# Kernel optimization log

Measured on AMD Instinct MI355X. Metric: run time of the kernel, lower is better.

## Reference

```python
import jax, jax.numpy as jnp
import numpy as np

EPS = 1e-6

def wave_repr(x, global_mode):
    # x: [B,S,D]
    x = jnp.clip(x, -10.0, 10.0)
    xsq = x * x
    if global_mode:
        Gsq = jnp.sum(xsq, axis=(1, 2), keepdims=True) + EPS  # [B,1,1]
    else:
        Gsq = jnp.sum(xsq, axis=1, keepdims=True) + EPS       # [B,1,D]
    G = jnp.maximum(jnp.sqrt(Gsq), EPS)
    # NOTE: source uses torch.div(..., rounding_mode='floor') -> floor division
    ratio = jnp.clip(jnp.floor(x / G), -0.99, 0.99)
    sqrt_term = jnp.sqrt(jnp.maximum(1.0 - ratio * ratio, EPS))
    alpha = jnp.arctan2(sqrt_term, ratio)
    return G * jnp.cos(alpha), G * jnp.sin(alpha)

def gelu(x):
    return jax.nn.gelu(x, approximate=False)

def rmsnorm(x, w):
    return x * jax.lax.rsqrt(jnp.mean(x * x, axis=-1, keepdims=True) + EPS) * w

def setup_inputs() -> dict:
    key = jax.random.key(0)
    B, S, D = 4, 4096, 1024
    ks = jax.random.split(key, 16)
    s = 0.02
    p = {
        'x': jax.random.normal(ks[0], (B, S, D), jnp.float32),
        'Wa': jax.random.normal(ks[1], (D, D)) * s, 'ba': jnp.zeros((D,)),
        'Wp': jax.random.normal(ks[2], (D, D)) * s, 'bp': jnp.zeros((D,)),
        'gate_bias': jnp.zeros((D,)),
        'w1r': jax.random.normal(ks[3], (D, 4 * D)) * s, 'b1r': jnp.zeros((4 * D,)),
        'w2r': jax.random.normal(ks[4], (4 * D, D)) * s, 'b2r': jnp.zeros((D,)),
        'w1i': jax.random.normal(ks[5], (D, 4 * D)) * s, 'b1i': jnp.zeros((4 * D,)),
        'w2i': jax.random.normal(ks[6], (4 * D, D)) * s, 'b2i': jnp.zeros((D,)),
        'We': jax.random.normal(ks[7], (2 * D, D)) * s, 'be': jnp.zeros((D,)),
        'g_rms': jnp.ones((D,)),
        'wf1': jax.random.normal(ks[8], (D, 2 * D)) * s, 'bf1': jnp.zeros((2 * D,)),
        'wf2': jax.random.normal(ks[9], (2 * D, D)) * s, 'bf2': jnp.zeros((D,)),
    }
    return p

def reference(x, Wa, ba, Wp, bp, gate_bias, w1r, b1r, w2r, b2r, w1i, b1i, w2i, b2i, We, be, g_rms, wf1, bf1, wf2, bf2):
    # wave representations: global (sentence) + local (token)
    rs, is_ = wave_repr(x, True)
    rt, it = wave_repr(x, False)
    cr = rs + rt
    ci = is_ + it
    # amplitude / phase
    amp = jnp.sqrt(cr * cr + ci * ci + EPS)
    ph = jnp.arctan2(ci, cr)
    # biological noise gate (eval mode: no noise)
    gate = jax.nn.sigmoid(amp @ Wa + ba + ph @ Wp + bp + gate_bias)
    gr = cr * gate
    gi = ci * gate
    rp = gelu(gr @ w1r + b1r) @ w2r + b2r
    ip = gelu(gi @ w1i + b1i) @ w2i + b2i
    # combine to embedding + RMSNorm
    wave = jnp.concatenate([rp, ip], axis=-1) @ We + be
    out = rmsnorm(wave, g_rms)
    y = gelu(out @ wf1 + bf1) @ wf2 + bf2
    return y
```

## Files before the change

### kernel.cpp

```cpp
#include <hip/hip_runtime.h>
#include <cmath>

typedef _Float16 f16;
typedef _Float16 f16x8 __attribute__((ext_vector_type(8)));
typedef _Float16 f16x4 __attribute__((ext_vector_type(4)));
typedef float f32x4 __attribute__((ext_vector_type(4)));

#define EPSF 1e-6f

__device__ __forceinline__ void gload16(const f16* g, const f16* l) {
  __builtin_amdgcn_global_load_lds(
      (__attribute__((address_space(1))) void*)g,
      (__attribute__((address_space(3))) void*)l, 16, 0, 0);
}

__device__ __forceinline__ float fast_gelu(float u) {
  const float z = u * 0.70710678118654752f;
  const float az = fabsf(z);
  const float t = __builtin_amdgcn_rcpf(fmaf(0.3275911f, az, 1.0f));
  float p = 1.061405429f;
  p = fmaf(p, t, -1.453152027f);
  p = fmaf(p, t, 1.421413741f);
  p = fmaf(p, t, -0.284496736f);
  p = fmaf(p, t, 0.254829592f);
  p = p * t;
  const float e = __expf(-az * az);
  float er = fmaf(-p, e, 1.0f);
  er = copysignf(er, z);
  return 0.5f * u * (1.0f + er);
}

__global__ void wtr_k(const float* __restrict__ W, f16* __restrict__ WT, int K, int N) {
  __shared__ float t[32][33];
  const int nb = blockIdx.x * 32, kb = blockIdx.y * 32;
  const int tx = threadIdx.x, ty = threadIdx.y;
#pragma unroll
  for (int i = ty; i < 32; i += 8) t[i][tx] = W[(size_t)(kb + i) * N + nb + tx];
  __syncthreads();
#pragma unroll
  for (int i = ty; i < 32; i += 8) WT[(size_t)(nb + i) * K + kb + tx] = (f16)t[tx][i];
}

__global__ void cast_k(const float* __restrict__ W, f16* __restrict__ H) {
  const size_t i = (size_t)blockIdx.x * 256 + threadIdx.x;
  const float4 v = ((const float4*)W)[i];
  f16x4 o;
  o[0] = (f16)v.x; o[1] = (f16)v.y; o[2] = (f16)v.z; o[3] = (f16)v.w;
  ((f16x4*)H)[i] = o;
}

__global__ void colsq_k(const float* __restrict__ x, float* __restrict__ part) {
  const int d = blockIdx.x * 256 + threadIdx.x;
  const int sb = blockIdx.y;
  const int b = blockIdx.z;
  const float* p = x + ((size_t)b * 4096 + (size_t)sb * 256) * 1024 + d;
  float acc = 0.f;
#pragma unroll 4
  for (int s = 0; s < 256; ++s) {
    float v = p[(size_t)s * 1024];
    v = fminf(fmaxf(v, -10.f), 10.f);
    acc = fmaf(v, v, acc);
  }
  part[((size_t)b * 16 + sb) * 1024 + d] = acc;
}

__global__ void stats_k(const float* __restrict__ part, float* __restrict__ Gsum,
                        float* __restrict__ amp) {
  const int b = blockIdx.x;
  const int t = threadIdx.x;
  __shared__ double red[256];
  float cs[4];
  double tot = 0.0;
#pragma unroll
  for (int i = 0; i < 4; ++i) {
    const int d = t + i * 256;
    double s = 0.0;
    for (int k = 0; k < 16; ++k) s += (double)part[((size_t)b * 16 + k) * 1024 + d];
    cs[i] = (float)s;
    tot += s;
  }
  red[t] = tot;
  __syncthreads();
  for (int st = 128; st > 0; st >>= 1) {
    if (t < st) red[t] += red[t + st];
    __syncthreads();
  }
  const float Gs = fmaxf(sqrtf((float)red[0] + EPSF), EPSF);
#pragma unroll
  for (int i = 0; i < 4; ++i) {
    const int d = t + i * 256;
    const float Gt = fmaxf(sqrtf(cs[i] + EPSF), EPSF);
    const float gs = Gs + Gt;
    Gsum[(b << 10) + d] = gs;
    amp[(b << 10) + d] = sqrtf(gs * gs + EPSF);
  }
}

__global__ void rowterm_k(const float* __restrict__ amp, const float* __restrict__ Wa,
                          const float* __restrict__ ba, const float* __restrict__ bp,
                          const float* __restrict__ gbias, float* __restrict__ rt) {
  const int b = blockIdx.y;
  const int d = blockIdx.x * 256 + threadIdx.x;
  const float* a = amp + (b << 10);
  double acc = 0.0;
  for (int k = 0; k < 1024; ++k) acc += (double)a[k] * (double)Wa[((size_t)k << 10) + d];
  rt[(b << 10) + d] = (float)acc + ba[d] + bp[d] + gbias[d];
}

__global__ void bc_k(const float* __restrict__ b2r, const float* __restrict__ b2i,
                     const float* __restrict__ We, const float* __restrict__ be,
                     float* __restrict__ bc) {
  const int n = blockIdx.x * 256 + threadIdx.x;
  double a = 0.0;
  for (int j = 0; j < 1024; ++j) a += (double)b2r[j] * (double)We[(size_t)j * 1024 + n];
  for (int j = 0; j < 1024; ++j)
    a += (double)b2i[j] * (double)We[(size_t)(1024 + j) * 1024 + n];
  bc[n] = (float)a + be[n];
}

__global__ void ph_k(const float* __restrict__ x, f16* __restrict__ ph, float phPos,
                     float phNeg) {
  const size_t i = (size_t)blockIdx.x * 256 + threadIdx.x;
  const float4 v = ((const float4*)x)[i];
  f16x4 o;
  o[0] = (f16)(v.x < 0.f ? phNeg : phPos);
  o[1] = (f16)(v.y < 0.f ? phNeg : phPos);
  o[2] = (f16)(v.z < 0.f ? phNeg : phPos);
  o[3] = (f16)(v.w < 0.f ? phNeg : phPos);
  ((f16x4*)ph)[i] = o;
}

__global__ void rms_k(const float* __restrict__ wave, const float* __restrict__ g,
                      f16* __restrict__ o) {
  const size_t row = blockIdx.x;
  const int t = threadIdx.x;
  const float4 v = ((const float4*)(wave + row * 1024))[t];
  float ss = v.x * v.x + v.y * v.y + v.z * v.z + v.w * v.w;
#pragma unroll
  for (int s = 32; s > 0; s >>= 1) ss += __shfl_down(ss, s);
  __shared__ float red[4];
  if ((t & 63) == 0) red[t >> 6] = ss;
  __syncthreads();
  const float tot = red[0] + red[1] + red[2] + red[3];
  const float r = rsqrtf(tot * (1.f / 1024.f) + EPSF);
  const float4 gv = ((const float4*)g)[t];
  f16x4 ov;
  ov[0] = (f16)(v.x * r * gv.x);
  ov[1] = (f16)(v.y * r * gv.y);
  ov[2] = (f16)(v.z * r * gv.z);
  ov[3] = (f16)(v.w * r * gv.w);
  ((f16x4*)(o + row * 1024))[t] = ov;
}

template <int EPI>
__global__ __launch_bounds__(512, 4) void gemm2_k(
    const f16* __restrict__ A, int lda, const f16* __restrict__ BT, int ldb, int K,
    const float* __restrict__ bias, float* __restrict__ outF, f16* __restrict__ outH,
    int ldo, const f16* __restrict__ phm, const float* __restrict__ rowterm,
    const float* __restrict__ Gsum, f16* __restrict__ gr, f16* __restrict__ gi, int r0,
    float ratioNeg, float stNeg) {
  __shared__ __align__(16) char smem[49152];
  f16(*smA)[4096] = reinterpret_cast<f16(*)[4096]>(smem);
  f16(*smB)[8192] = reinterpret_cast<f16(*)[8192]>(smem + 16384);
  const int tid = threadIdx.x;
  const int w = tid >> 6, l = tid & 63;

  const int ncol = gridDim.y;
  const int bid = blockIdx.x * ncol + blockIdx.y;
  const int nwg = gridDim.x * ncol;
  const int q = nwg >> 3, rr = nwg & 7;
  const int xcd = bid & 7, idx = bid >> 3;
  const int swz = (xcd < rr ? xcd * (q + 1) : rr * (q + 1) + (xcd - rr) * q) + idx;
  const int bx = swz / ncol, by = swz % ncol;
  const size_t rbase = (size_t)bx * 128;
  const size_t cbase = (size_t)by * 256;

  const int srow = (w << 4) + (l >> 2);
  const int slot = l & 3;
  const int ssA = ((slot ^ ((srow >> 1) & 3)) << 3);

  f32x4 acc[4][4];
  const f32x4 zero = {0.f, 0.f, 0.f, 0.f};
#pragma unroll
  for (int m = 0; m < 4; ++m)
#pragma unroll
    for (int n = 0; n < 4; ++n) acc[m][n] = zero;

  const f16* gA = A + (rbase + srow) * (size_t)lda + ssA;
  const f16* gB0 = BT + (cbase + srow) * (size_t)ldb + ssA;
  const int srow1 = srow + 128;
  const f16* gB1 = BT + (cbase + srow1) * (size_t)ldb + ((slot ^ ((srow1 >> 1) & 3)) << 3);

  const int nk = K >> 5;
  auto stage = [&](int buf, size_t ko) {
    gload16(gA + ko, &smA[buf][w << 9]);
    gload16(gB0 + ko, &smB[buf][w << 9]);
    gload16(gB1 + ko, &smB[buf][4096 + (w << 9)]);
  };
  stage(0, 0);
  __syncthreads();

  const int arow = l & 15;
  const int kg = (((l >> 4) ^ ((arow >> 1) & 3)) << 3);
  const int wr = (w >> 2) << 6;
  const int wc = (w & 3) << 6;

  for (int t = 0; t < nk; ++t) {
    const int cur = t & 1;
    if (t + 1 < nk) stage(cur ^ 1, (size_t)(t + 1) << 5);
    const f16* ap = &smA[cur][(wr + arow) * 32 + kg];
    const f16* bp = &smB[cur][(wc + arow) * 32 + kg];
    f16x8 af[4], bf[4];
#pragma unroll
    for (int m = 0; m < 4; ++m) af[m] = *(const f16x8*)(ap + m * 512);
#pragma unroll
    for (int n = 0; n < 4; ++n) bf[n] = *(const f16x8*)(bp + n * 512);
#pragma unroll
    for (int m = 0; m < 4; ++m)
#pragma unroll
      for (int n = 0; n < 4; ++n)
        acc[m][n] = __builtin_amdgcn_mfma_f32_16x16x32_f16(af[m], bf[n], acc[m][n], 0, 0, 0);
    __syncthreads();
  }

  const int fr = l & 15, hi = l >> 4;
  const int r4 = hi << 2;

  if constexpr (EPI == 3 || EPI == 5) {
    float* ep = reinterpret_cast<float*>(smem + w * 4352);
#pragma unroll
    for (int m = 0; m < 4; ++m) {
#pragma unroll
      for (int n = 0; n < 4; ++n) {
        const int cl = n * 16 + fr;
#pragma unroll
        for (int j = 0; j < 4; ++j) {
          float v = acc[m][n][j];
          if constexpr (EPI == 3) v = fast_gelu(v + bias[cbase + wc + cl]);
          ep[(r4 + j) * 68 + cl] = v;
        }
      }
      asm volatile("s_waitcnt lgkmcnt(0)" ::: "memory");
      __builtin_amdgcn_sched_barrier(0);
#pragma unroll
      for (int it = 0; it < 2; ++it) {
        const int rl = l >> 2;
        const int ch = (l & 3) + it * 4;
        const float* pr = &ep[rl * 68 + ch * 8];
        f16x8 o;
#pragma unroll
        for (int e = 0; e < 8; ++e) o[e] = (f16)pr[e];
        *(f16x8*)&outH[(rbase + wr + m * 16 + rl) * (size_t)ldo + (cbase + wc + ch * 8)] = o;
      }
      asm volatile("s_waitcnt lgkmcnt(0)" ::: "memory");
      __builtin_amdgcn_sched_barrier(0);
    }
  } else {
#pragma unroll
    for (int m = 0; m < 4; ++m) {
#pragma unroll
      for (int n = 0; n < 4; ++n) {
        const size_t col = cbase + wc + n * 16 + fr;
#pragma unroll
        for (int j = 0; j < 4; ++j) {
          const size_t row = rbase + wr + m * 16 + r4 + j;
          const float v = acc[m][n][j];
          if constexpr (EPI == 0) {
            outF[row * (size_t)ldo + col] = v + bias[col];
          } else if constexpr (EPI == 1) {
            outF[row * (size_t)ldo + col] += v;
          } else if constexpr (EPI == 4) {
            const int gb = (int)(((size_t)r0 + row) >> 12);
            const float pre = v + rowterm[((size_t)gb << 10) + col];
            const float gate = __builtin_amdgcn_rcpf(1.f + __expf(-pre));
            const float ph = (float)phm[row * 1024 + col];
            const bool neg = ph > 2.f;
            const float gs = Gsum[((size_t)gb << 10) + col];
            const float cr = neg ? gs * ratioNeg : 0.f;
            const float ci = gs * (neg ? stNeg : 1.f);
            gr[row * 1024 + col] = (f16)(cr * gate);
            gi[row * 1024 + col] = (f16)(ci * gate);
          }
        }
      }
    }
  }
}

extern "C" void kernel_launch(void* const* d_in, const int* in_sizes, int n_in,
                              void* d_out, int out_size, void* d_ws, size_t ws_size,
                              hipStream_t stream) {
  const float* x     = (const float*)d_in[0];
  const float* Wa    = (const float*)d_in[1];
  const float* ba    = (const float*)d_in[2];
  const float* Wp    = (const float*)d_in[3];
  const float* bp    = (const float*)d_in[4];
  const float* gbias = (const float*)d_in[5];
  const float* w1r   = (const float*)d_in[6];
  const float* b1r   = (const float*)d_in[7];
  const float* w2r   = (const float*)d_in[8];
  const float* b2r   = (const float*)d_in[9];
  const float* w1i   = (const float*)d_in[10];
  const float* b1i   = (const float*)d_in[11];
  const float* w2i   = (const float*)d_in[12];
  const float* b2i   = (const float*)d_in[13];
  const float* We    = (const float*)d_in[14];
  const float* be    = (const float*)d_in[15];
  const float* grms  = (const float*)d_in[16];
  const float* wf1   = (const float*)d_in[17];
  const float* bf1   = (const float*)d_in[18];
  const float* wf2   = (const float*)d_in[19];
  const float* bf2   = (const float*)d_in[20];
  float* out = (float*)d_out;

  char* ws = (char*)d_ws;
  size_t off = 0;
  auto alloc = [&](size_t bytes) -> void* {
    void* p = (void*)(ws + off);
    off += (bytes + 255) & ~(size_t)255;
    return p;
  };

  f16* WpT   = (f16*)alloc((size_t)1024 * 1024 * 2);
  f16* w1rT  = (f16*)alloc((size_t)4096 * 1024 * 2);
  f16* w1iT  = (f16*)alloc((size_t)4096 * 1024 * 2);
  f16* wf1T  = (f16*)alloc((size_t)2048 * 1024 * 2);
  f16* wf2T  = (f16*)alloc((size_t)1024 * 2048 * 2);
  f16* WcrT  = (f16*)alloc((size_t)1024 * 4096 * 2);
  f16* WciT  = (f16*)alloc((size_t)1024 * 4096 * 2);
  float* part    = (float*)alloc((size_t)4 * 16 * 1024 * 4);
  float* GsumB   = (float*)alloc((size_t)4 * 1024 * 4);
  float* ampB    = (float*)alloc((size_t)4 * 1024 * 4);
  float* rowterm = (float*)alloc((size_t)4 * 1024 * 4);
  float* bcB     = (float*)alloc((size_t)1024 * 4);
  const size_t staticEnd = off;

  char* tmp = ws + staticEnd;
  f16* WeT  = (f16*)tmp;
  f16* w2rH = (f16*)(tmp + (size_t)4 * 1024 * 1024);
  f16* w2iH = (f16*)(tmp + (size_t)12 * 1024 * 1024);

  {
    dim3 b(32, 8);
    wtr_k<<<dim3(32, 32), b, 0, stream>>>(Wp, WpT, 1024, 1024);
    wtr_k<<<dim3(128, 32), b, 0, stream>>>(w1r, w1rT, 1024, 4096);
    wtr_k<<<dim3(128, 32), b, 0, stream>>>(w1i, w1iT, 1024, 4096);
    wtr_k<<<dim3(64, 32), b, 0, stream>>>(wf1, wf1T, 1024, 2048);
    wtr_k<<<dim3(32, 64), b, 0, stream>>>(wf2, wf2T, 2048, 1024);
    wtr_k<<<dim3(32, 64), b, 0, stream>>>(We, WeT, 2048, 1024);
    cast_k<<<dim3(4096), 256, 0, stream>>>(w2r, w2rH);
    cast_k<<<dim3(4096), 256, 0, stream>>>(w2i, w2iH);
  }

  colsq_k<<<dim3(4, 16, 4), 256, 0, stream>>>(x, part);
  stats_k<<<4, 256, 0, stream>>>(part, GsumB, ampB);
  rowterm_k<<<dim3(4, 4), 256, 0, stream>>>(ampB, Wa, ba, bp, gbias, rowterm);
  bc_k<<<dim3(4), 256, 0, stream>>>(b2r, b2i, We, be, bcB);

  gemm2_k<5><<<dim3(8, 16), 512, 0, stream>>>(WeT, 2048, w2rH, 1024, 1024, nullptr,
      nullptr, WcrT, 4096, nullptr, nullptr, nullptr, nullptr, nullptr, 0, 0.f, 0.f);
  gemm2_k<5><<<dim3(8, 16), 512, 0, stream>>>(WeT + 1024, 2048, w2iH, 1024, 1024, nullptr,
      nullptr, WciT, 4096, nullptr, nullptr, nullptr, nullptr, nullptr, 0, 0.f, 0.f);

  const float ratioNeg = -0.99f;
  const float stNeg = sqrtf(fmaxf(1.0f - 0.99f * 0.99f, EPSF));
  const float phPos = atan2f(1.0f, 0.0f);
  const float phNeg = atan2f(stNeg, ratioNeg);

  const long Ntok = (long)in_sizes[0] / 1024;
  const size_t perRow = 14336;
  long R = (long)((ws_size > staticEnd ? ws_size - staticEnd : 0) / perRow);
  R &= ~255L;
  if (R > 8192) R = 8192;
  if (R < 256) R = 256;

  char* cb = ws + staticEnd;
  f16* phB = (f16*)cb;
  f16* grB = (f16*)(cb + (size_t)R * 2048);
  f16* giB = (f16*)(cb + (size_t)R * 4096);
  f16* h1B = (f16*)(cb + (size_t)R * 6144);
  float* waveF = (float*)phB;
  f16* outB = giB;
  f16* h2B = h1B;

  for (long r0 = 0; r0 < Ntok; r0 += R) {
    const long Rc = (Ntok - r0 < R) ? (Ntok - r0) : R;
    const int gm = (int)(Rc / 128);
    ph_k<<<dim3((int)Rc), 256, 0, stream>>>(x + r0 * 1024, phB, phPos, phNeg);
    gemm2_k<4><<<dim3(gm, 4), 512, 0, stream>>>(phB, 1024, WpT, 1024, 1024, nullptr,
        nullptr, nullptr, 1024, phB, rowterm, GsumB, grB, giB, (int)r0, ratioNeg, stNeg);
    gemm2_k<3><<<dim3(gm, 16), 512, 0, stream>>>(grB, 1024, w1rT, 1024, 1024, b1r,
        nullptr, h1B, 4096, nullptr, nullptr, nullptr, nullptr, nullptr, 0, 0.f, 0.f);
    gemm2_k<0><<<dim3(gm, 4), 512, 0, stream>>>(h1B, 4096, WcrT, 4096, 4096, bcB,
        waveF, nullptr, 1024, nullptr, nullptr, nullptr, nullptr, nullptr, 0, 0.f, 0.f);
    gemm2_k<3><<<dim3(gm, 16), 512, 0, stream>>>(giB, 1024, w1iT, 1024, 1024, b1i,
        nullptr, h1B, 4096, nullptr, nullptr, nullptr, nullptr, nullptr, 0, 0.f, 0.f);
    gemm2_k<1><<<dim3(gm, 4), 512, 0, stream>>>(h1B, 4096, WciT, 4096, 4096, nullptr,
        waveF, nullptr, 1024, nullptr, nullptr, nullptr, nullptr, nullptr, 0, 0.f, 0.f);
    rms_k<<<dim3((int)Rc), 256, 0, stream>>>(waveF, grms, outB);
    gemm2_k<3><<<dim3(gm, 8), 512, 0, stream>>>(outB, 1024, wf1T, 1024, 1024, bf1,
        nullptr, h2B, 2048, nullptr, nullptr, nullptr, nullptr, nullptr, 0, 0.f, 0.f);
    gemm2_k<0><<<dim3(gm, 4), 512, 0, stream>>>(h2B, 2048, wf2T, 2048, 2048, bf2,
        out + r0 * 1024, nullptr, 1024, nullptr, nullptr, nullptr, nullptr, nullptr, 0, 0.f, 0.f);
  }
}
```

Before: 1.368 ms.

## Use 128x128-tile GEMM for N=1024 outputs and split-K the small row-term matvecs

Adds a second GEMM kernel with 128x128 tiles and 256 threads, used for every GEMM whose output width is 1024 (gate, the two wave projections, final FFN). This doubles the workgroup count on those launches so the GPU is better filled. The gate epilogue now goes through LDS so the gr/gi stores are vectorized. The serial double-precision matvecs for the row term and the combined bias are split over K into partial kernels plus reduce kernels, which raises parallelism at the cost of extra launches and scratch buffers. The smaller tiles lower per-block data reuse.

New measurement: 1.487 ms. +8.7%, slower.

```diff
diff --git a/kernel.cpp b/kernel.cpp
--- a/kernel.cpp
+++ b/kernel.cpp
@@ -96,26 +96,49 @@
   }
 }
 
-__global__ void rowterm_k(const float* __restrict__ amp, const float* __restrict__ Wa,
-                          const float* __restrict__ ba, const float* __restrict__ bp,
-                          const float* __restrict__ gbias, float* __restrict__ rt) {
+__global__ void rtp_k(const float* __restrict__ amp, const float* __restrict__ Wa,
+                      double* __restrict__ part) {
+  const int d = blockIdx.x * 256 + threadIdx.x;
   const int b = blockIdx.y;
-  const int d = blockIdx.x * 256 + threadIdx.x;
+  const int kc = blockIdx.z;
   const float* a = amp + (b << 10);
   double acc = 0.0;
-  for (int k = 0; k < 1024; ++k) acc += (double)a[k] * (double)Wa[((size_t)k << 10) + d];
+  for (int jj = 0; jj < 128; ++jj) {
+    const int k = kc * 128 + jj;
+    acc += (double)a[k] * (double)Wa[((size_t)k << 10) + d];
+  }
+  part[(((size_t)b * 8 + kc) << 10) + d] = acc;
+}
+__global__ void rtr_k(const double* __restrict__ part, const float* __restrict__ ba,
+                      const float* __restrict__ bp, const float* __restrict__ gbias,
+                      float* __restrict__ rt) {
+  const int d = blockIdx.x * 256 + threadIdx.x;
+  const int b = blockIdx.y;
+  double acc = 0.0;
+#pragma unroll
+  for (int kc = 0; kc < 8; ++kc) acc += part[(((size_t)b * 8 + kc) << 10) + d];
   rt[(b << 10) + d] = (float)acc + ba[d] + bp[d] + gbias[d];
 }
 
-__global__ void bc_k(const float* __restrict__ b2r, const float* __restrict__ b2i,
-                     const float* __restrict__ We, const float* __restrict__ be,
-                     float* __restrict__ bc) {
+__global__ void bcp_k(const float* __restrict__ b2r, const float* __restrict__ b2i,
+                      const float* __restrict__ We, double* __restrict__ part) {
   const int n = blockIdx.x * 256 + threadIdx.x;
-  double a = 0.0;
-  for (int j = 0; j < 1024; ++j) a += (double)b2r[j] * (double)We[(size_t)j * 1024 + n];
-  for (int j = 0; j < 1024; ++j)
-    a += (double)b2i[j] * (double)We[(size_t)(1024 + j) * 1024 + n];
-  bc[n] = (float)a + be[n];
+  const int kc = blockIdx.y;
+  double acc = 0.0;
+  for (int jj = 0; jj < 128; ++jj) {
+    const int j = kc * 128 + jj;
+    const float bv = (j < 1024) ? b2r[j] : b2i[j - 1024];
+    acc += (double)bv * (double)We[(size_t)j * 1024 + n];
+  }
+  part[((size_t)kc << 10) + n] = acc;
+}
+__global__ void bcr_k(const double* __restrict__ part, const float* __restrict__ be,
+                      float* __restrict__ bc) {
+  const int n = blockIdx.x * 256 + threadIdx.x;
+  double acc = 0.0;
+#pragma unroll
+  for (int kc = 0; kc < 16; ++kc) acc += part[((size_t)kc << 10) + n];
+  bc[n] = (float)acc + be[n];
 }
 
 __global__ void ph_k(const float* __restrict__ x, f16* __restrict__ ph, float phPos,
@@ -155,10 +178,7 @@
 template <int EPI>
 __global__ __launch_bounds__(512, 4) void gemm2_k(
     const f16* __restrict__ A, int lda, const f16* __restrict__ BT, int ldb, int K,
-    const float* __restrict__ bias, float* __restrict__ outF, f16* __restrict__ outH,
-    int ldo, const f16* __restrict__ phm, const float* __restrict__ rowterm,
-    const float* __restrict__ Gsum, f16* __restrict__ gr, f16* __restrict__ gi, int r0,
-    float ratioNeg, float stNeg) {
+    const float* __restrict__ bias, f16* __restrict__ outH, int ldo) {
   __shared__ __align__(16) char smem[49152];
   f16(*smA)[4096] = reinterpret_cast<f16(*)[4096]>(smem);
   f16(*smB)[8192] = reinterpret_cast<f16(*)[8192]>(smem + 16384);
@@ -177,7 +197,7 @@
 
   const int srow = (w << 4) + (l >> 2);
   const int slot = l & 3;
-  const int ssA = ((slot ^ ((srow >> 1) & 3)) << 3);
+  const int ss = ((slot ^ ((srow >> 1) & 3)) << 3);
 
   f32x4 acc[4][4];
   const f32x4 zero = {0.f, 0.f, 0.f, 0.f};
@@ -186,10 +206,9 @@
 #pragma unroll
     for (int n = 0; n < 4; ++n) acc[m][n] = zero;
 
-  const f16* gA = A + (rbase + srow) * (size_t)lda + ssA;
-  const f16* gB0 = BT + (cbase + srow) * (size_t)ldb + ssA;
-  const int srow1 = srow + 128;
-  const f16* gB1 = BT + (cbase + srow1) * (size_t)ldb + ((slot ^ ((srow1 >> 1) & 3)) << 3);
+  const f16* gA = A + (rbase + srow) * (size_t)lda + ss;
+  const f16* gB0 = BT + (cbase + srow) * (size_t)ldb + ss;
+  const f16* gB1 = BT + (cbase + srow + 128) * (size_t)ldb + ss;
 
   const int nk = K >> 5;
   auto stage = [&](int buf, size_t ko) {
@@ -225,35 +244,153 @@
 
   const int fr = l & 15, hi = l >> 4;
   const int r4 = hi << 2;
-
-  if constexpr (EPI == 3 || EPI == 5) {
-    float* ep = reinterpret_cast<float*>(smem + w * 4352);
+  float* ep = reinterpret_cast<float*>(smem + w * 4352);
+#pragma unroll
+  for (int m = 0; m < 4; ++m) {
+#pragma unroll
+    for (int n = 0; n < 4; ++n) {
+      const int cl = n * 16 + fr;
+#pragma unroll
+      for (int j = 0; j < 4; ++j) {
+        float v = acc[m][n][j];
+        if constexpr (EPI == 3) v = fast_gelu(v + bias[cbase + wc + cl]);
+        ep[(r4 + j) * 68 + cl] = v;
+      }
+    }
+    asm volatile("s_waitcnt lgkmcnt(0)" ::: "memory");
+    __builtin_amdgcn_sched_barrier(0);
+#pragma unroll
+    for (int it = 0; it < 2; ++it) {
+      const int rl = l >> 2;
+      const int ch = (l & 3) + it * 4;
+      const float* pr = &ep[rl * 68 + ch * 8];
+      f16x8 o;
+#pragma unroll
+      for (int e = 0; e < 8; ++e) o[e] = (f16)pr[e];
+      *(f16x8*)&outH[(rbase + wr + m * 16 + rl) * (size_t)ldo + (cbase + wc + ch * 8)] = o;
+    }
+    asm volatile("s_waitcnt lgkmcnt(0)" ::: "memory");
+    __builtin_amdgcn_sched_barrier(0);
+  }
+}
+
+template <int EPI>
+__global__ __launch_bounds__(256, 5) void gemm1_k(
+    const f16* __restrict__ A, int lda, const f16* __restrict__ BT, int ldb, int K,
+    const float* __restrict__ bias, float* __restrict__ outF, int ldo,
+    const f16* __restrict__ phm, const float* __restrict__ rowterm,
+    const float* __restrict__ Gsum, f16* __restrict__ gr, f16* __restrict__ gi, int r0,
+    float ratioNeg, float stNeg) {
+  __shared__ __align__(16) char smem[32768];
+  f16(*smA)[4096] = reinterpret_cast<f16(*)[4096]>(smem);
+  f16(*smB)[4096] = reinterpret_cast<f16(*)[4096]>(smem + 16384);
+  const int tid = threadIdx.x;
+  const int wv = tid >> 6, ln = tid & 63;
+
+  const int ncol = gridDim.y;
+  const int bid = blockIdx.x * ncol + blockIdx.y;
+  const int nwg = gridDim.x * ncol;
+  const int q = nwg >> 3, rr = nwg & 7;
+  const int xcd = bid & 7, idx = bid >> 3;
+  const int swz = (xcd < rr ? xcd * (q + 1) : rr * (q + 1) + (xcd - rr) * q) + idx;
+  const int bx = swz / ncol, by = swz % ncol;
+  const size_t rbase = (size_t)bx * 128;
+  const size_t cbase = (size_t)by * 128;
+
+  const int srow = (wv << 4) + (ln >> 2);
+  const int slot = ln & 3;
+  const int ss = ((slot ^ ((srow >> 1) & 3)) << 3);
+
+  f32x4 acc[4][4];
+  const f32x4 zero = {0.f, 0.f, 0.f, 0.f};
+#pragma unroll
+  for (int m = 0; m < 4; ++m)
+#pragma unroll
+    for (int n = 0; n < 4; ++n) acc[m][n] = zero;
+
+  const f16* gA = A + (rbase + srow) * (size_t)lda + ss;
+  const f16* gB = BT + (cbase + srow) * (size_t)ldb + ss;
+
+  const int nk = K >> 5;
+  auto stage = [&](int buf, size_t ko) {
+    gload16(gA + ko, &smA[buf][wv << 9]);
+    gload16(gA + ko + (size_t)64 * lda, &smA[buf][2048 + (wv << 9)]);
+    gload16(gB + ko, &smB[buf][wv << 9]);
+    gload16(gB + ko + (size_t)64 * ldb, &smB[buf][2048 + (wv << 9)]);
+  };
+  stage(0, 0);
+  __syncthreads();
+
+  const int arow = ln & 15;
+  const int kg = (((ln >> 4) ^ ((arow >> 1) & 3)) << 3);
+  const int wr = (wv >> 1) << 6;
+  const int wc = (wv & 1) << 6;
+
+  for (int t = 0; t < nk; ++t) {
+    const int cur = t & 1;
+    if (t + 1 < nk) stage(cur ^ 1, (size_t)(t + 1) << 5);
+    const f16* ap = &smA[cur][(wr + arow) * 32 + kg];
+    const f16* bp = &smB[cur][(wc + arow) * 32 + kg];
+    f16x8 af[4], bf[4];
+#pragma unroll
+    for (int m = 0; m < 4; ++m) af[m] = *(const f16x8*)(ap + m * 512);
+#pragma unroll
+    for (int n = 0; n < 4; ++n) bf[n] = *(const f16x8*)(bp + n * 512);
+#pragma unroll
+    for (int m = 0; m < 4; ++m)
+#pragma unroll
+      for (int n = 0; n < 4; ++n)
+        acc[m][n] = __builtin_amdgcn_mfma_f32_16x16x32_f16(af[m], bf[n], acc[m][n], 0, 0, 0);
+    __syncthreads();
+  }
+
+  const int fr = ln & 15, hi = ln >> 4;
+  const int r4 = hi << 2;
+
+  if constexpr (EPI == 4) {
+    float* ep = reinterpret_cast<float*>(smem + wv * 4352);
 #pragma unroll
     for (int m = 0; m < 4; ++m) {
+      float grv[4][4], giv[4][4];
 #pragma unroll
       for (int n = 0; n < 4; ++n) {
-        const int cl = n * 16 + fr;
+        const size_t col = cbase + wc + n * 16 + fr;
 #pragma unroll
         for (int j = 0; j < 4; ++j) {
-          float v = acc[m][n][j];
-          if constexpr (EPI == 3) v = fast_gelu(v + bias[cbase + wc + cl]);
-          ep[(r4 + j) * 68 + cl] = v;
+          const size_t row = rbase + wr + m * 16 + r4 + j;
+          const int gb = (int)(((size_t)r0 + row) >> 12);
+          const float pre = acc[m][n][j] + rowterm[((size_t)gb << 10) + col];
+          const float gate = __builtin_amdgcn_rcpf(1.f + __expf(-pre));
+          const float ph = (float)phm[row * 1024 + col];
+          const bool neg = ph > 2.f;
+          const float gs = Gsum[((size_t)gb << 10) + col];
+          grv[n][j] = (neg ? gs * ratioNeg : 0.f) * gate;
+          giv[n][j] = gs * (neg ? stNeg : 1.f) * gate;
         }
       }
-      asm volatile("s_waitcnt lgkmcnt(0)" ::: "memory");
-      __builtin_amdgcn_sched_barrier(0);
-#pragma unroll
-      for (int it = 0; it < 2; ++it) {
-        const int rl = l >> 2;
-        const int ch = (l & 3) + it * 4;
-        const float* pr = &ep[rl * 68 + ch * 8];
-        f16x8 o;
-#pragma unroll
-        for (int e = 0; e < 8; ++e) o[e] = (f16)pr[e];
-        *(f16x8*)&outH[(rbase + wr + m * 16 + rl) * (size_t)ldo + (cbase + wc + ch * 8)] = o;
+#pragma unroll
+      for (int pass = 0; pass < 2; ++pass) {
+        f16* dst = pass ? gi : gr;
+#pragma unroll
+        for (int n = 0; n < 4; ++n)
+#pragma unroll
+          for (int j = 0; j < 4; ++j)
+            ep[(r4 + j) * 68 + n * 16 + fr] = pass ? giv[n][j] : grv[n][j];
+        asm volatile("s_waitcnt lgkmcnt(0)" ::: "memory");
+        __builtin_amdgcn_sched_barrier(0);
+#pragma unroll
+        for (int it = 0; it < 2; ++it) {
+          const int rl = ln >> 2;
+          const int ch = (ln & 3) + it * 4;
+          const float* pr = &ep[rl * 68 + ch * 8];
+          f16x8 o;
+#pragma unroll
+          for (int e = 0; e < 8; ++e) o[e] = (f16)pr[e];
+          *(f16x8*)&dst[(rbase + wr + m * 16 + rl) * 1024 + (cbase + wc + ch * 8)] = o;
+        }
+        asm volatile("s_waitcnt lgkmcnt(0)" ::: "memory");
+        __builtin_amdgcn_sched_barrier(0);
       }
-      asm volatile("s_waitcnt lgkmcnt(0)" ::: "memory");
-      __builtin_amdgcn_sched_barrier(0);
     }
   } else {
 #pragma unroll
@@ -267,19 +404,8 @@
           const float v = acc[m][n][j];
           if constexpr (EPI == 0) {
             outF[row * (size_t)ldo + col] = v + bias[col];
-          } else if constexpr (EPI == 1) {
+          } else {
             outF[row * (size_t)ldo + col] += v;
-          } else if constexpr (EPI == 4) {
-            const int gb = (int)(((size_t)r0 + row) >> 12);
-            const float pre = v + rowterm[((size_t)gb << 10) + col];
-            const float gate = __builtin_amdgcn_rcpf(1.f + __expf(-pre));
-            const float ph = (float)phm[row * 1024 + col];
-            const bool neg = ph > 2.f;
-            const float gs = Gsum[((size_t)gb << 10) + col];
-            const float cr = neg ? gs * ratioNeg : 0.f;
-            const float ci = gs * (neg ? stNeg : 1.f);
-            gr[row * 1024 + col] = (f16)(cr * gate);
-            gi[row * 1024 + col] = (f16)(ci * gate);
           }
         }
       }
@@ -333,6 +459,8 @@
   float* ampB    = (float*)alloc((size_t)4 * 1024 * 4);
   float* rowterm = (float*)alloc((size_t)4 * 1024 * 4);
   float* bcB     = (float*)alloc((size_t)1024 * 4);
+  double* rtPart = (double*)alloc((size_t)4 * 8 * 1024 * 8);
+  double* bcPart = (double*)alloc((size_t)16 * 1024 * 8);
   const size_t staticEnd = off;
 
   char* tmp = ws + staticEnd;
@@ -354,13 +482,15 @@
 
   colsq_k<<<dim3(4, 16, 4), 256, 0, stream>>>(x, part);
   stats_k<<<4, 256, 0, stream>>>(part, GsumB, ampB);
-  rowterm_k<<<dim3(4, 4), 256, 0, stream>>>(ampB, Wa, ba, bp, gbias, rowterm);
-  bc_k<<<dim3(4), 256, 0, stream>>>(b2r, b2i, We, be, bcB);
+  rtp_k<<<dim3(4, 4, 8), 256, 0, stream>>>(ampB, Wa, rtPart);
+  rtr_k<<<dim3(4, 4), 256, 0, stream>>>(rtPart, ba, bp, gbias, rowterm);
+  bcp_k<<<dim3(4, 16), 256, 0, stream>>>(b2r, b2i, We, bcPart);
+  bcr_k<<<dim3(4), 256, 0, stream>>>(bcPart, be, bcB);
 
   gemm2_k<5><<<dim3(8, 16), 512, 0, stream>>>(WeT, 2048, w2rH, 1024, 1024, nullptr,
-      nullptr, WcrT, 4096, nullptr, nullptr, nullptr, nullptr, nullptr, 0, 0.f, 0.f);
+      WcrT, 4096);
   gemm2_k<5><<<dim3(8, 16), 512, 0, stream>>>(WeT + 1024, 2048, w2iH, 1024, 1024, nullptr,
-      nullptr, WciT, 4096, nullptr, nullptr, nullptr, nullptr, nullptr, 0, 0.f, 0.f);
+      WciT, 4096);
 
   const float ratioNeg = -0.99f;
   const float stNeg = sqrtf(fmaxf(1.0f - 0.99f * 0.99f, EPSF));
@@ -387,20 +517,20 @@
     const long Rc = (Ntok - r0 < R) ? (Ntok - r0) : R;
     const int gm = (int)(Rc / 128);
     ph_k<<<dim3((int)Rc), 256, 0, stream>>>(x + r0 * 1024, phB, phPos, phNeg);
-    gemm2_k<4><<<dim3(gm, 4), 512, 0, stream>>>(phB, 1024, WpT, 1024, 1024, nullptr,
-        nullptr, nullptr, 1024, phB, rowterm, GsumB, grB, giB, (int)r0, ratioNeg, stNeg);
+    gemm1_k<4><<<dim3(gm, 8), 256, 0, stream>>>(phB, 1024, WpT, 1024, 1024, nullptr,
+        nullptr, 1024, phB, rowterm, GsumB, grB, giB, (int)r0, ratioNeg, stNeg);
     gemm2_k<3><<<dim3(gm, 16), 512, 0, stream>>>(grB, 1024, w1rT, 1024, 1024, b1r,
-        nullptr, h1B, 4096, nullptr, nullptr, nullptr, nullptr, nullptr, 0, 0.f, 0.f);
-    gemm2_k<0><<<dim3(gm, 4), 512, 0, stream>>>(h1B, 4096, WcrT, 4096, 4096, bcB,
-        waveF, nullptr, 1024, nullptr, nullptr, nullptr, nullptr, nullptr, 0, 0.f, 0.f);
+        h1B, 4096);
+    gemm1_k<0><<<dim3(gm, 8), 256, 0, stream>>>(h1B, 4096, WcrT, 4096, 4096, bcB,
+        waveF, 1024, nullptr, nullptr, nullptr, nullptr, nullptr, 0, 0.f, 0.f);
     gemm2_k<3><<<dim3(gm, 16), 512, 0, stream>>>(giB, 1024, w1iT, 1024, 1024, b1i,
-        nullptr, h1B, 4096, nullptr, nullptr, nullptr, nullptr, nullptr, 0, 0.f, 0.f);
-    gemm2_k<1><<<dim3(gm, 4), 512, 0, stream>>>(h1B, 4096, WciT, 4096, 4096, nullptr,
-        waveF, nullptr, 1024, nullptr, nullptr, nullptr, nullptr, nullptr, 0, 0.f, 0.f);
+        h1B, 4096);
+    gemm1_k<1><<<dim3(gm, 8), 256, 0, stream>>>(h1B, 4096, WciT, 4096, 4096, nullptr,
+        waveF, 1024, nullptr, nullptr, nullptr, nullptr, nullptr, 0, 0.f, 0.f);
     rms_k<<<dim3((int)Rc), 256, 0, stream>>>(waveF, grms, outB);
     gemm2_k<3><<<dim3(gm, 8), 512, 0, stream>>>(outB, 1024, wf1T, 1024, 1024, bf1,
-        nullptr, h2B, 2048, nullptr, nullptr, nullptr, nullptr, nullptr, 0, 0.f, 0.f);
-    gemm2_k<0><<<dim3(gm, 4), 512, 0, stream>>>(h2B, 2048, wf2T, 2048, 2048, bf2,
-        out + r0 * 1024, nullptr, 1024, nullptr, nullptr, nullptr, nullptr, nullptr, 0, 0.f, 0.f);
-  }
-}
+        h2B, 2048);
+    gemm1_k<0><<<dim3(gm, 8), 256, 0, stream>>>(h2B, 2048, wf2T, 2048, 2048, bf2,
+        out + r0 * 1024, 1024, nullptr, nullptr, nullptr, nullptr, nullptr, 0, 0.f, 0.f);
+  }
+}
```
